# Kernel optimization log

Measured on AMD Instinct MI355X. Metric: run time of the kernel, lower is better.

## Reference

```python
import jax, jax.numpy as jnp
import numpy as np

H = 8  # num_heads

def setup_inputs() -> dict:
    key = jax.random.key(0)
    ks = jax.random.split(key, 10)
    B, N, D, E = 1, 4096, 256, 65536
    s = 0.02
    return {
        "x": jax.random.normal(ks[0], (B, N, D), jnp.float32),
        "edge_index": jax.random.randint(ks[1], (2, E), 0, N, jnp.int32),
        "edge_attr": jax.random.normal(ks[2], (E, 3), jnp.float32),
        "Wq": jax.random.normal(ks[3], (D, D), jnp.float32) * s,
        "bq": jnp.zeros((D,), jnp.float32),
        "Wk": jax.random.normal(ks[4], (D, D), jnp.float32) * s,
        "bk": jnp.zeros((D,), jnp.float32),
        "Wv": jax.random.normal(ks[5], (D, D), jnp.float32) * s,
        "bv": jnp.zeros((D,), jnp.float32),
        "Wo": jax.random.normal(ks[6], (D, D), jnp.float32) * s,
        "bo": jnp.zeros((D,), jnp.float32),
        "We": jax.random.normal(ks[7], (3, H), jnp.float32) * s,
        "be": jnp.zeros((H,), jnp.float32),
    }

def reference(x, edge_index, edge_attr, Wq, bq, Wk, bk, Wv, bv, Wo, bo, We, be):
    B, N, D = x.shape
    hd = D // H
    q = (x @ Wq + bq).reshape(B, N, H, hd)
    k = (x @ Wk + bk).reshape(B, N, H, hd)
    v = (x @ Wv + bv).reshape(B, N, H, hd)
    # scores: [B, H, N, N]
    scores = jnp.einsum("bihd,bjhd->bhij", q, k) / jnp.sqrt(jnp.asarray(hd, x.dtype))
    # edge bias: torch scatter_ writes a row-constant value into column edge_tgt
    # for every query row (edge_src unused in the original). Equivalent to a
    # per-head column bias [H, N], broadcast over batch and query rows.
    eb = edge_attr @ We + be            # [E, H]
    edge_tgt = edge_index[1]
    col_bias = jnp.zeros((H, N), x.dtype).at[:, edge_tgt].set(eb.T)  # [H, N]
    scores = scores + col_bias[None, :, None, :]
    attn = jax.nn.softmax(scores, axis=-1)
    out = jnp.einsum("bhij,bjhd->bihd", attn, v).reshape(B, N, D)
    return out @ Wo + bo
```

## Files before the change

kernel.cpp:

```cpp
#include <hip/hip_runtime.h>
#include <hip/hip_bf16.h>
#include <math.h>

#define NUM_H 8
#define HD 32
#define DD 256
#define NSPLIT 4

typedef __attribute__((ext_vector_type(8))) short bf16x8;
typedef __attribute__((ext_vector_type(4))) float f32x4;

__device__ __forceinline__ unsigned short f2b(float f) {
  unsigned u = __builtin_bit_cast(unsigned, f);
  u += 0x7FFFu + ((u >> 16) & 1u);
  return (unsigned short)(u >> 16);
}

__device__ __forceinline__ unsigned pack2(float a, float b) {
  float2 t; t.x = a; t.y = b;
  __hip_bfloat162 r = __float22bfloat162_rn(t);
  unsigned u;
  __builtin_memcpy(&u, &r, sizeof(u));
  return u;
}

#define LOG2E 1.4426950408889634f


__global__ void sel_scatter_kernel(const int* __restrict__ tgt, int* __restrict__ sel, int E) {
  int e = blockIdx.x * 256 + threadIdx.x;
  if (e < E) atomicMax(&sel[tgt[e]], e);
}

__global__ void cvt_all(const float* __restrict__ W0, const float* __restrict__ W1,
                        const float* __restrict__ W2, const float* __restrict__ W3,
                        unsigned short* __restrict__ T0, unsigned short* __restrict__ T1,
                        unsigned short* __restrict__ T2, unsigned short* __restrict__ T3,
                        const float* __restrict__ x, unsigned short* __restrict__ xf,
                        int* __restrict__ sel, int N) {
  const int z = blockIdx.z;
  const int tid = threadIdx.x;
  if (z == 5) {
    const int b = blockIdx.x * 8 + blockIdx.y;
    if (b < (N + 255) / 256) {
      int t = b * 256 + tid;
      if (t < N) sel[t] = -1;
    }
    return;
  }
  if (z == 4) {
    const int b = blockIdx.x * 8 + blockIdx.y;
    const int ntiles = N / 16;
    for (int tt = 0; tt < ntiles / 64; ++tt) {
      const int t4 = b * (ntiles / 64) + tt;
#pragma unroll
      for (int gi = 0; gi < 2; ++gi) {
        const int g = tid + gi * 256;
        const int lr = g >> 5, kk = (g >> 2) & 7, lg = g & 3;
        const float* src = x + ((size_t)t4 * 16 + lr) * DD + kk * 32 + lg * 8;
        const float4 a = *reinterpret_cast<const float4*>(src);
        const float4 c = *reinterpret_cast<const float4*>(src + 4);
        uint4 o;
        o.x = pack2(a.x, a.y); o.y = pack2(a.z, a.w);
        o.z = pack2(c.x, c.y); o.w = pack2(c.z, c.w);
        *reinterpret_cast<uint4*>(xf + (size_t)t4 * 4096 + kk * 512 + lg * 128 + lr * 8) = o;
      }
    }
    return;
  }
  __shared__ float t[32][33];
  const float* W = (z == 0) ? W0 : (z == 1) ? W1 : (z == 2) ? W2 : W3;
  unsigned short* WF = (z == 0) ? T0 : (z == 1) ? T1 : (z == 2) ? T2 : T3;
  const int bx = blockIdx.x, by = blockIdx.y;
  const int lx = tid & 31, ly = tid >> 5;
#pragma unroll
  for (int r = 0; r < 32; r += 8)
    t[r + ly][lx] = W[(size_t)(bx * 32 + r + ly) * DD + by * 32 + lx];
  __syncthreads();
  if (tid < 128) {
    const int ct = tid & 31, lg = tid >> 5;
    bf16x8 val;
#pragma unroll
    for (int e = 0; e < 8; ++e)
      val[e] = (short)f2b(t[lg * 8 + e][ct]);
    const int off = (by * 8 + bx) * 1024 + (ct >> 4) * 512 + lg * 128 + (ct & 15) * 8;
    *reinterpret_cast<bf16x8*>(WF + off) = val;
  }
}

__global__ __launch_bounds__(256) void proj_qkv(const unsigned short* __restrict__ Xf,
                                                const unsigned short* __restrict__ WTq,
                                                const unsigned short* __restrict__ WTk,
                                                const unsigned short* __restrict__ WTv,
                                                const float* __restrict__ bq,
                                                const float* __restrict__ bk,
                                                const float* __restrict__ bv,
                                                unsigned short* __restrict__ qfrag,
                                                unsigned short* __restrict__ kfrag,
                                                unsigned short* __restrict__ vfrag,
                                                const int* __restrict__ sel,
                                                const float* __restrict__ ea,
                                                const float* __restrict__ We,
                                                const float* __restrict__ be,
                                                float* __restrict__ biasg, int N) {
  const int z = blockIdx.z;
  const int tid = threadIdx.x;
  if (z == 3) {
    const int b = blockIdx.x * 8 + blockIdx.y;
    if (b >= (N + 255) / 256) return;
    const int t = b * 256 + tid;
    if (t >= N) return;
    int e = sel[t];
    bool has = (e >= 0);
    float a0 = 0.f, a1 = 0.f, a2 = 0.f;
    if (has) {
      a0 = ea[3 * (size_t)e];
      a1 = ea[3 * (size_t)e + 1];
      a2 = ea[3 * (size_t)e + 2];
    }
#pragma unroll
    for (int h = 0; h < NUM_H; ++h) {
      float v = has ? (a0 * We[h] + a1 * We[NUM_H + h] + a2 * We[2 * NUM_H + h] + be[h]) : 0.f;
      biasg[(size_t)h * N + t] = v * LOG2E;
    }
    return;
  }
  const unsigned short* WT = (z == 0) ? WTq : (z == 1) ? WTk : WTv;
  const float* bias = (z == 0) ? bq : (z == 1) ? bk : bv;
  const int w = tid >> 6, l = tid & 63;
  const int lr = l & 15, lg = l >> 4;
  const int nt = blockIdx.x * 4 + w;
  const int n0 = nt * 16;
  const int cb = blockIdx.y;
  const int c0 = cb * 32;
  const int NT = N / 16;
  const f32x4 zero4 = {0.f, 0.f, 0.f, 0.f};
  f32x4 acc0 = zero4, acc1 = zero4;
  const unsigned short* ap = Xf + (size_t)nt * 4096 + lg * 128 + lr * 8;
  const unsigned short* bp = WT + (size_t)cb * 8192 + lg * 128 + lr * 8;
  if (z < 2) {
#pragma unroll
    for (int kk = 0; kk < 8; ++kk) {
      bf16x8 a  = *reinterpret_cast<const bf16x8*>(ap + kk * 512);
      bf16x8 b0 = *reinterpret_cast<const bf16x8*>(bp + kk * 1024);
      bf16x8 b1 = *reinterpret_cast<const bf16x8*>(bp + kk * 1024 + 512);
      acc0 = __builtin_amdgcn_mfma_f32_16x16x32_bf16(b0, a, acc0, 0, 0, 0);
      acc1 = __builtin_amdgcn_mfma_f32_16x16x32_bf16(b1, a, acc1, 0, 0, 0);
    }
    const f32x4 bv0 = *reinterpret_cast<const f32x4*>(bias + c0 + lg * 4);
    const f32x4 bv1 = *reinterpret_cast<const f32x4*>(bias + c0 + 16 + lg * 4);
    const float qs = (z == 0) ? (0.17677669529663687f * LOG2E) : 1.0f;
    unsigned short* QK = z ? kfrag : qfrag;
    size_t base;
    int rowoff;
    if (z == 1) {
      const int j = ((nt & 3) << 4) + lr;
      const int pos = ((j >> 5) * 2 + ((j >> 2) & 1)) * 16 + (((j & 31) >> 3) << 2) + (j & 3);
      const int t16p = ((nt >> 2) << 2) + (pos >> 4);
      base = ((size_t)cb * NT + t16p) * 512;
      rowoff = (pos & 15) * 8;
    } else {
      base = ((size_t)cb * NT + nt) * 512;
      rowoff = lr * 8;
    }
    const int kf0 = (lg >> 1) * 128, ke = (lg & 1) * 4;
    uint2 o0, o1;
    o0.x = pack2((acc0[0] + bv0[0]) * qs, (acc0[1] + bv0[1]) * qs);
    o0.y = pack2((acc0[2] + bv0[2]) * qs, (acc0[3] + bv0[3]) * qs);
    o1.x = pack2((acc1[0] + bv1[0]) * qs, (acc1[1] + bv1[1]) * qs);
    o1.y = pack2((acc1[2] + bv1[2]) * qs, (acc1[3] + bv1[3]) * qs);
    *reinterpret_cast<uint2*>(QK + base + kf0 + rowoff + ke) = o0;
    *reinterpret_cast<uint2*>(QK + base + 256 + kf0 + rowoff + ke) = o1;
  } else {
#pragma unroll
    for (int kk = 0; kk < 8; ++kk) {
      bf16x8 a  = *reinterpret_cast<const bf16x8*>(ap + kk * 512);
      bf16x8 b0 = *reinterpret_cast<const bf16x8*>(bp + kk * 1024);
      bf16x8 b1 = *reinterpret_cast<const bf16x8*>(bp + kk * 1024 + 512);
      acc0 = __builtin_amdgcn_mfma_f32_16x16x32_bf16(a, b0, acc0, 0, 0, 0);
      acc1 = __builtin_amdgcn_mfma_f32_16x16x32_bf16(a, b1, acc1, 0, 0, 0);
    }
    const float bc0 = bias[c0 + lr], bc1 = bias[c0 + 16 + lr];
    const int lgf = ((n0 & 16) >> 3) + (lg >> 1);
    const int ke = (lg & 1) * 4;
    const size_t vbase = ((size_t)cb * (N / 32) + (n0 >> 5)) * 1024;
    uint2 o0, o1;
    o0.x = pack2(acc0[0] + bc0, acc0[1] + bc0);
    o0.y = pack2(acc0[2] + bc0, acc0[3] + bc0);
    o1.x = pack2(acc1[0] + bc1, acc1[1] + bc1);
    o1.y = pack2(acc1[2] + bc1, acc1[3] + bc1);
    *reinterpret_cast<uint2*>(vfrag + vbase + lgf * 128 + lr * 8 + ke) = o0;
    *reinterpret_cast<uint2*>(vfrag + vbase + 512 + lgf * 128 + lr * 8 + ke) = o1;
  }
}

__global__ __launch_bounds__(256) void proj_out(const unsigned short* __restrict__ Obf,
                                                const unsigned short* __restrict__ WT,
                                                const float* __restrict__ bias,
                                                float* __restrict__ Y, int N) {
  const int w = threadIdx.x >> 6, l = threadIdx.x & 63;
  const int lr = l & 15, lg = l >> 4;
  const int nt = blockIdx.x * 4 + w;
  const int n0 = nt * 16;
  const int cb = blockIdx.y;
  const int c0 = cb * 32;
  const f32x4 zero4 = {0.f, 0.f, 0.f, 0.f};
  f32x4 acc0 = zero4, acc1 = zero4;
  const unsigned short* ap = Obf + (size_t)nt * 4096 + lg * 128 + lr * 8;
  const unsigned short* bp = WT + (size_t)cb * 8192 + lg * 128 + lr * 8;
#pragma unroll
  for (int kk = 0; kk < 8; ++kk) {
    bf16x8 a  = *reinterpret_cast<const bf16x8*>(ap + kk * 512);
    bf16x8 b0 = *reinterpret_cast<const bf16x8*>(bp + kk * 1024);
    bf16x8 b1 = *reinterpret_cast<const bf16x8*>(bp + kk * 1024 + 512);
    acc0 = __builtin_amdgcn_mfma_f32_16x16x32_bf16(a, b0, acc0, 0, 0, 0);
    acc1 = __builtin_amdgcn_mfma_f32_16x16x32_bf16(a, b1, acc1, 0, 0, 0);
  }
  const float bc0 = bias[c0 + lr], bc1 = bias[c0 + 16 + lr];
#pragma unroll
  for (int r = 0; r < 4; ++r) {
    Y[(size_t)(n0 + lg * 4 + r) * DD + c0 + lr]      = acc0[r] + bc0;
    Y[(size_t)(n0 + lg * 4 + r) * DD + c0 + 16 + lr] = acc1[r] + bc1;
  }
}

__global__ __launch_bounds__(256, 4) void attn_mfma(const unsigned short* __restrict__ qfrag,
                                                    const unsigned short* __restrict__ kfrag,
                                                    const unsigned short* __restrict__ vfrag,
                                                    const float* __restrict__ biasg,
                                                    float* __restrict__ Opart,
                                                    float* __restrict__ lpart, int N) {
  __shared__ float Bs[1024];
  const int tid = threadIdx.x;
  const int w = tid >> 6, l = tid & 63;
  const int lr = l & 15, lg = l >> 4;
  const int bid = blockIdx.x;
  const int h = bid & 7;
  const int rem = bid >> 3;
  const int qblk = rem & 31;
  const int s = rem >> 5;
  const int q0 = qblk * 128 + w * 32;
  const int NT = N / 16;
  const int jlo = s * (N / NSPLIT);

  const bf16x8 qfA = *reinterpret_cast<const bf16x8*>(
      qfrag + ((size_t)h * NT + (q0 >> 4)) * 512 + l * 8);
  const bf16x8 qfB = *reinterpret_cast<const bf16x8*>(
      qfrag + ((size_t)h * NT + (q0 >> 4) + 1) * 512 + l * 8);

  *reinterpret_cast<float4*>(&Bs[tid * 4]) =
      *reinterpret_cast<const float4*>(biasg + (size_t)h * N + jlo + tid * 4);
  __syncthreads();

  const unsigned short* kb_ = kfrag + ((size_t)h * NT + (jlo >> 4)) * 512 + l * 8;
  const unsigned short* vb_ = vfrag + ((size_t)h * (N / 32) + (jlo >> 5)) * 1024 + l * 8;

  float lsA = 0.f, lsB = 0.f;
  const f32x4 zero4 = {0.f, 0.f, 0.f, 0.f};
  f32x4 oA0 = zero4, oA1 = zero4, oB0 = zero4, oB1 = zero4;

#define LOADK(dst, t)                                                               \
  {                                                                                 \
    _Pragma("unroll") for (int jf = 0; jf < 4; ++jf)                                \
        dst[jf] = *reinterpret_cast<const bf16x8*>(kb_ + ((t) * 4 + jf) * 512);     \
  }
#define LOADV(dst, t)                                                               \
  {                                                                                 \
    _Pragma("unroll") for (int cd = 0; cd < 4; ++cd)                                \
        dst[cd] = *reinterpret_cast<const bf16x8*>(vb_ + ((t) * 2 + (cd >> 1)) * 1024 \
                                                   + (cd & 1) * 512);               \
  }

  const int ntiles = (N / NSPLIT) >> 6;
  bf16x8 kf[4], vf[4];
  LOADK(kf, 0);
  for (int t = 0; t < ntiles; ++t) {
    __builtin_amdgcn_s_barrier();

    LOADV(vf, t);
    const int tbase = t * 64;

    f32x4 b4[4];
#pragma unroll
    for (int jf = 0; jf < 4; ++jf)
      b4[jf] = *reinterpret_cast<const f32x4*>(
          &Bs[tbase + (jf >> 1) * 32 + lg * 8 + (jf & 1) * 4]);

    f32x4 scA[4];
    __builtin_amdgcn_s_setprio(1);
#pragma unroll
    for (int jf = 0; jf < 4; ++jf)
      scA[jf] = __builtin_amdgcn_mfma_f32_16x16x32_bf16(kf[jf], qfA, b4[jf], 0, 0, 0);
    __builtin_amdgcn_s_setprio(0);

    unsigned pkA[8];
    float rA = 0.f;
#pragma unroll
    for (int jf = 0; jf < 4; ++jf) {
      float a0 = __builtin_amdgcn_exp2f(scA[jf][0]);
      float a1 = __builtin_amdgcn_exp2f(scA[jf][1]);
      float a2 = __builtin_amdgcn_exp2f(scA[jf][2]);
      float a3 = __builtin_amdgcn_exp2f(scA[jf][3]);
      rA += (a0 + a1) + (a2 + a3);
      pkA[jf * 2]     = pack2(a0, a1);
      pkA[jf * 2 + 1] = pack2(a2, a3);
    }
    lsA += rA;

    f32x4 scB[4];
    __builtin_amdgcn_s_setprio(1);
#pragma unroll
    for (int jf = 0; jf < 4; ++jf)
      scB[jf] = __builtin_amdgcn_mfma_f32_16x16x32_bf16(kf[jf], qfB, b4[jf], 0, 0, 0);
    __builtin_amdgcn_s_setprio(0);

    if (t + 1 < ntiles) LOADK(kf, t + 1);

    unsigned pkB[8];
    float rB = 0.f;
#pragma unroll
    for (int jf = 0; jf < 4; ++jf) {
      float c0 = __builtin_amdgcn_exp2f(scB[jf][0]);
      float c1 = __builtin_amdgcn_exp2f(scB[jf][1]);
      float c2 = __builtin_amdgcn_exp2f(scB[jf][2]);
      float c3 = __builtin_amdgcn_exp2f(scB[jf][3]);
      rB += (c0 + c1) + (c2 + c3);
      pkB[jf * 2]     = pack2(c0, c1);
      pkB[jf * 2 + 1] = pack2(c2, c3);
    }
    lsB += rB;

    bf16x8 pA0, pA1, pB0, pB1;
    __builtin_memcpy(&pA0, &pkA[0], 16);
    __builtin_memcpy(&pA1, &pkA[4], 16);
    __builtin_memcpy(&pB0, &pkB[0], 16);
    __builtin_memcpy(&pB1, &pkB[4], 16);
    __builtin_amdgcn_s_setprio(1);
    oA0 = __builtin_amdgcn_mfma_f32_16x16x32_bf16(pA0, vf[0], oA0, 0, 0, 0);
    oA1 = __builtin_amdgcn_mfma_f32_16x16x32_bf16(pA0, vf[1], oA1, 0, 0, 0);
    oB0 = __builtin_amdgcn_mfma_f32_16x16x32_bf16(pB0, vf[0], oB0, 0, 0, 0);
    oB1 = __builtin_amdgcn_mfma_f32_16x16x32_bf16(pB0, vf[1], oB1, 0, 0, 0);
    oA0 = __builtin_amdgcn_mfma_f32_16x16x32_bf16(pA1, vf[2], oA0, 0, 0, 0);
    oA1 = __builtin_amdgcn_mfma_f32_16x16x32_bf16(pA1, vf[3], oA1, 0, 0, 0);
    oB0 = __builtin_amdgcn_mfma_f32_16x16x32_bf16(pB1, vf[2], oB0, 0, 0, 0);
    oB1 = __builtin_amdgcn_mfma_f32_16x16x32_bf16(pB1, vf[3], oB1, 0, 0, 0);
    __builtin_amdgcn_s_setprio(0);
  }
#undef LOADK
#undef LOADV

  lsA += __shfl_xor(lsA, 16);
  lsA += __shfl_xor(lsA, 32);
  lsB += __shfl_xor(lsB, 16);
  lsB += __shfl_xor(lsB, 32);

  const size_t srow = ((size_t)s * NUM_H + h) * N;
  if (lg == 0) {
    lpart[srow + q0 + lr]      = lsA;
    lpart[srow + q0 + 16 + lr] = lsB;
  }
  float* ObA = Opart + (srow + q0) * 32;
  float* ObB = Opart + (srow + q0 + 16) * 32;
#pragma unroll
  for (int r = 0; r < 4; ++r) {
    ObA[(size_t)(lg * 4 + r) * 32 + lr]      = oA0[r];
    ObA[(size_t)(lg * 4 + r) * 32 + 16 + lr] = oA1[r];
    ObB[(size_t)(lg * 4 + r) * 32 + lr]      = oB0[r];
    ObB[(size_t)(lg * 4 + r) * 32 + 16 + lr] = oB1[r];
  }
}

__global__ __launch_bounds__(256) void combine_kernel(const float* __restrict__ Op,
                                                      const float* __restrict__ lp,
                                                      unsigned short* __restrict__ obf, int N) {
  const int idx = blockIdx.x * 256 + threadIdx.x;
  const int d4 = idx & 7;
  const int row = idx >> 3;
  const size_t HN = (size_t)NUM_H * N;
  float wsum = 0.f;
#pragma unroll
  for (int s = 0; s < NSPLIT; ++s) wsum += lp[s * HN + row];
  const float inv = 1.f / wsum;
  float4 acc = make_float4(0.f, 0.f, 0.f, 0.f);
#pragma unroll
  for (int s = 0; s < NSPLIT; ++s) {
    const float4 v = *reinterpret_cast<const float4*>(Op + (s * HN + row) * 32 + d4 * 4);
    acc.x += v.x; acc.y += v.y; acc.z += v.z; acc.w += v.w;
  }
  const int h = row / N, n = row - h * N;
  uint2 o;
  o.x = pack2(acc.x * inv, acc.y * inv);
  o.y = pack2(acc.z * inv, acc.w * inv);
  const int off = (n >> 4) * 4096 + h * 512 + (d4 >> 1) * 128 + (n & 15) * 8 + (d4 & 1) * 4;
  *reinterpret_cast<uint2*>(obf + off) = o;
}

extern "C" void kernel_launch(void* const* d_in, const int* in_sizes, int n_in,
                              void* d_out, int out_size, void* d_ws, size_t ws_size,
                              hipStream_t stream) {
  const float* x  = (const float*)d_in[0];
  const int* eidx = (const int*)d_in[1];
  const float* ea = (const float*)d_in[2];
  const float* Wq = (const float*)d_in[3];
  const float* bq = (const float*)d_in[4];
  const float* Wk = (const float*)d_in[5];
  const float* bk = (const float*)d_in[6];
  const float* Wv = (const float*)d_in[7];
  const float* bv = (const float*)d_in[8];
  const float* Wo = (const float*)d_in[9];
  const float* bo = (const float*)d_in[10];
  const float* We = (const float*)d_in[11];
  const float* be = (const float*)d_in[12];
  float* out = (float*)d_out;

  const int N = in_sizes[0] / DD;
  const int E = in_sizes[1] / 2;
  const int* tgt = eidx + E;

  unsigned short* xf    = (unsigned short*)d_ws;
  unsigned short* qfrag = xf    + (size_t)N * DD;
  unsigned short* kfrag = qfrag + (size_t)N * DD;
  unsigned short* vfrag = kfrag + (size_t)N * DD;
  unsigned short* obf   = vfrag + (size_t)N * DD;
  unsigned short* WTq   = obf   + (size_t)N * DD;
  unsigned short* WTk = WTq + DD * DD;
  unsigned short* WTv = WTk + DD * DD;
  unsigned short* WTo = WTv + DD * DD;
  float* bias  = (float*)(WTo + DD * DD);
  float* Opart = bias + (size_t)NUM_H * N;
  float* lpart = Opart + (size_t)NSPLIT * NUM_H * N * 32;
  int*   sel   = (int*)(lpart + (size_t)NSPLIT * NUM_H * N);

  dim3 cg(8, 8, 6);
  cvt_all<<<cg, 256, 0, stream>>>(Wq, Wk, Wv, Wo, WTq, WTk, WTv, WTo, x, xf, sel, N);

  sel_scatter_kernel<<<(E + 255) / 256, 256, 0, stream>>>(tgt, sel, E);

  dim3 pg(N / 64, DD / 32, 4);
  proj_qkv<<<pg, 256, 0, stream>>>(xf, WTq, WTk, WTv, bq, bk, bv, qfrag, kfrag, vfrag,
                                   sel, ea, We, be, bias, N);

  attn_mfma<<<(N / 128) * NUM_H * NSPLIT, 256, 0, stream>>>(qfrag, kfrag, vfrag, bias,
                                                            Opart, lpart, N);

  combine_kernel<<<(NUM_H * N * 8) / 256, 256, 0, stream>>>(Opart, lpart, obf, N);

  dim3 og(N / 64, DD / 32);
  proj_out<<<og, 256, 0, stream>>>(obf, WTo, bo, out, N);
}
```

Baseline: 64.31 us.

## Store attention partials as bf16 fragments and drop per-tile barrier

The split-K attention kernel now packs its unnormalized partial outputs to bf16 and writes them straight in MFMA fragment order with 16-byte stores, instead of scattering fp32 values. The combine kernel is rewritten to gather from that layout and sum the splits in fp32. This halves the partial-output traffic between the two kernels, at the cost of bf16 rounding of the partials and narrower 2-byte gathers in the combine step. The per-iteration s_barrier in the attention loop is also removed, which assumes the shared bias buffer is no longer written inside the loop.

```diff
diff --git a/kernel.cpp b/kernel.cpp
--- a/kernel.cpp
+++ b/kernel.cpp
@@ -22,6 +22,11 @@
   unsigned u;
   __builtin_memcpy(&u, &r, sizeof(u));
   return u;
+}
+
+__device__ __forceinline__ float b2f(unsigned short v) {
+  unsigned u = (unsigned)v << 16;
+  return __builtin_bit_cast(float, u);
 }
 
 #define LOG2E 1.4426950408889634f
@@ -228,7 +233,7 @@
                                                     const unsigned short* __restrict__ kfrag,
                                                     const unsigned short* __restrict__ vfrag,
                                                     const float* __restrict__ biasg,
-                                                    float* __restrict__ Opart,
+                                                    unsigned short* __restrict__ Opb,
                                                     float* __restrict__ lpart, int N) {
   __shared__ float Bs[1024];
   const int tid = threadIdx.x;
@@ -275,8 +280,6 @@
   bf16x8 kf[4], vf[4];
   LOADK(kf, 0);
   for (int t = 0; t < ntiles; ++t) {
-    __builtin_amdgcn_s_barrier();
-
     LOADV(vf, t);
     const int tbase = t * 64;
 
@@ -359,18 +362,20 @@
     lpart[srow + q0 + lr]      = lsA;
     lpart[srow + q0 + 16 + lr] = lsB;
   }
-  float* ObA = Opart + (srow + q0) * 32;
-  float* ObB = Opart + (srow + q0 + 16) * 32;
-#pragma unroll
-  for (int r = 0; r < 4; ++r) {
-    ObA[(size_t)(lg * 4 + r) * 32 + lr]      = oA0[r];
-    ObA[(size_t)(lg * 4 + r) * 32 + 16 + lr] = oA1[r];
-    ObB[(size_t)(lg * 4 + r) * 32 + lr]      = oB0[r];
-    ObB[(size_t)(lg * 4 + r) * 32 + 16 + lr] = oB1[r];
-  }
-}
-
-__global__ __launch_bounds__(256) void combine_kernel(const float* __restrict__ Op,
+  const size_t tile = (((size_t)s * NUM_H + h) * (N >> 5) + (q0 >> 5)) * 1024;
+  unsigned pk[8];
+  pk[0] = pack2(oA0[0], oA0[1]); pk[1] = pack2(oA0[2], oA0[3]);
+  pk[2] = pack2(oA1[0], oA1[1]); pk[3] = pack2(oA1[2], oA1[3]);
+  pk[4] = pack2(oB0[0], oB0[1]); pk[5] = pack2(oB0[2], oB0[3]);
+  pk[6] = pack2(oB1[0], oB1[1]); pk[7] = pack2(oB1[2], oB1[3]);
+  uint4 s0, s1;
+  __builtin_memcpy(&s0, &pk[0], 16);
+  __builtin_memcpy(&s1, &pk[4], 16);
+  *reinterpret_cast<uint4*>(Opb + tile + l * 16)     = s0;
+  *reinterpret_cast<uint4*>(Opb + tile + l * 16 + 8) = s1;
+}
+
+__global__ __launch_bounds__(256) void combine_kernel(const unsigned short* __restrict__ Opb,
                                                       const float* __restrict__ lp,
                                                       unsigned short* __restrict__ obf, int N) {
   const int idx = blockIdx.x * 256 + threadIdx.x;
@@ -381,16 +386,24 @@
 #pragma unroll
   for (int s = 0; s < NSPLIT; ++s) wsum += lp[s * HN + row];
   const float inv = 1.f / wsum;
-  float4 acc = make_float4(0.f, 0.f, 0.f, 0.f);
+  const int h = row / N, n = row - h * N;
+  const int qo = n & 31;
+  const int half = qo >> 4, lgq = (qo >> 2) & 3, r = qo & 3;
+  const int d0 = d4 * 4;
+  const int which = d0 >> 4, lr0 = d0 & 15;
+  const int fbase = (lgq * 16 + lr0) * 16 + half * 8 + which * 4 + r;
+  float acc0 = 0.f, acc1 = 0.f, acc2 = 0.f, acc3 = 0.f;
 #pragma unroll
   for (int s = 0; s < NSPLIT; ++s) {
-    const float4 v = *reinterpret_cast<const float4*>(Op + (s * HN + row) * 32 + d4 * 4);
-    acc.x += v.x; acc.y += v.y; acc.z += v.z; acc.w += v.w;
-  }
-  const int h = row / N, n = row - h * N;
+    const size_t tb = (((size_t)s * NUM_H + h) * (N >> 5) + (n >> 5)) * 1024;
+    acc0 += b2f(Opb[tb + fbase]);
+    acc1 += b2f(Opb[tb + fbase + 16]);
+    acc2 += b2f(Opb[tb + fbase + 32]);
+    acc3 += b2f(Opb[tb + fbase + 48]);
+  }
   uint2 o;
-  o.x = pack2(acc.x * inv, acc.y * inv);
-  o.y = pack2(acc.z * inv, acc.w * inv);
+  o.x = pack2(acc0 * inv, acc1 * inv);
+  o.y = pack2(acc2 * inv, acc3 * inv);
   const int off = (n >> 4) * 4096 + h * 512 + (d4 >> 1) * 128 + (n & 15) * 8 + (d4 & 1) * 4;
   *reinterpret_cast<uint2*>(obf + off) = o;
 }
@@ -427,8 +440,8 @@
   unsigned short* WTv = WTk + DD * DD;
   unsigned short* WTo = WTv + DD * DD;
   float* bias  = (float*)(WTo + DD * DD);
-  float* Opart = bias + (size_t)NUM_H * N;
-  float* lpart = Opart + (size_t)NSPLIT * NUM_H * N * 32;
+  unsigned short* Opb = (unsigned short*)(bias + (size_t)NUM_H * N);
+  float* lpart = (float*)(Opb + (size_t)NSPLIT * NUM_H * N * 32);
   int*   sel   = (int*)(lpart + (size_t)NSPLIT * NUM_H * N);
 
   dim3 cg(8, 8, 6);
@@ -441,9 +454,9 @@
                                    sel, ea, We, be, bias, N);
 
   attn_mfma<<<(N / 128) * NUM_H * NSPLIT, 256, 0, stream>>>(qfrag, kfrag, vfrag, bias,
-                                                            Opart, lpart, N);
-
-  combine_kernel<<<(NUM_H * N * 8) / 256, 256, 0, stream>>>(Opart, lpart, obf, N);
+                                                            Opb, lpart, N);
+
+  combine_kernel<<<(NUM_H * N * 8) / 256, 256, 0, stream>>>(Opb, lpart, obf, N);
 
   dim3 og(N / 64, DD / 32);
   proj_out<<<og, 256, 0, stream>>>(obf, WTo, bo, out, N);
```

Result: faster. 62.68 us (-2.5%).
